# Performance work log

Hardware: AMD Instinct MI355X
Metric: run time of the kernel (lower is better)

Reference implementation:

```python
import jax, jax.numpy as jnp
import numpy as np

NUM_CLASSES = 80
IOU_THR = 0.5
SCORE_THR = 0.3
K = 256              # per-class candidate pool (pre-NMS top-k)
MAX_PER_CLASS = 100  # max_output_size_per_class
MAX_TOTAL = 100      # max_total_size
NEG = -1e9


def _make_boxes(key, shape):
    kc, ks = jax.random.split(key)
    cyx = jax.random.uniform(kc, shape + (2,), dtype=jnp.float32)
    hw = jax.random.uniform(ks, shape + (2,), dtype=jnp.float32) * 0.2
    return jnp.concatenate([cyx - hw * 0.5, cyx + hw * 0.5], axis=-1)  # [y1,x1,y2,x2]


def setup_inputs() -> dict:
    key = jax.random.key(0)
    ks = jax.random.split(key, 9)
    B = 8
    inp = {}
    for i, g in enumerate([52, 26, 13]):
        inp[f"b{i+1}"] = _make_boxes(ks[3 * i], (B, g, g, 3))                       # (B,g,g,3,4)
        inp[f"c{i+1}"] = jax.random.uniform(ks[3 * i + 1], (B, g, g, 3, 1))          # objectness
        inp[f"p{i+1}"] = jax.random.uniform(ks[3 * i + 2], (B, g, g, 3, NUM_CLASSES))
    return inp


def _pairwise_iou(b):  # b: (K,4) in [y1,x1,y2,x2]
    y1, x1, y2, x2 = b[:, 0], b[:, 1], b[:, 2], b[:, 3]
    area = (y2 - y1) * (x2 - x1)
    iy = jnp.clip(jnp.minimum(y2[:, None], y2[None, :]) - jnp.maximum(y1[:, None], y1[None, :]), 0.0)
    ix = jnp.clip(jnp.minimum(x2[:, None], x2[None, :]) - jnp.maximum(x1[:, None], x1[None, :]), 0.0)
    inter = iy * ix
    union = area[:, None] + area[None, :] - inter
    return jnp.where(union > 0, inter / union, 0.0)


def _nms_one_class(boxes, scores):  # boxes (N,4), scores (N,)
    sc, idx = jax.lax.top_k(scores, K)
    b = boxes[idx]                      # (K,4) sorted by score desc
    valid = sc > SCORE_THR
    iou = _pairwise_iou(b)              # (K,K)
    rng = jnp.arange(K)

    def body(keep, i):
        cur = keep[i] & valid[i]
        keep = keep & ~(cur & (iou[i] > IOU_THR) & (rng > i))
        return keep, cur

    _, kept = jax.lax.scan(body, jnp.ones(K, dtype=bool), rng)
    kept = kept & (jnp.cumsum(kept) <= MAX_PER_CLASS)
    return b, jnp.where(kept, sc, NEG)  # (K,4), (K,)


def _combined_nms(boxes, scores):  # boxes (B,N,4), scores (B,N,C)
    per_class = jax.vmap(_nms_one_class, in_axes=(None, 1))   # over classes
    per_image = jax.vmap(per_class, in_axes=(0, 0))           # over batch
    cb, cs = per_image(boxes, scores)                         # (B,C,K,4), (B,C,K)
    B, C = scores.shape[0], scores.shape[2]
    flat_s = cs.reshape(B, C * K)
    flat_b = cb.reshape(B, C * K, 4)
    cls_ids = jnp.broadcast_to(jnp.arange(C, dtype=jnp.float32)[:, None], (C, K)).reshape(C * K)
    top_s, top_i = jax.lax.top_k(flat_s, MAX_TOTAL)           # global top-100
    top_b = jnp.take_along_axis(flat_b, top_i[:, :, None], axis=1)
    top_c = cls_ids[top_i]
    valid = top_s > SCORE_THR
    boxes_out = jnp.clip(jnp.where(valid[..., None], top_b, 0.0), 0.0, 1.0)  # clip_boxes=True
    scores_out = jnp.where(valid, top_s, 0.0)
    classes_out = jnp.where(valid, top_c, 0.0)
    nvalid = valid.sum(axis=-1).astype(jnp.int32)
    return boxes_out, scores_out, classes_out, nvalid


def reference(b1, c1, p1, b2, c2, p2, b3, c3, p3):
    B = b1.shape[0]
    bboxes = jnp.concatenate([b.reshape(B, -1, 4) for b in (b1, b2, b3)], axis=1)          # (B,N,4)
    conf = jnp.concatenate([c.reshape(B, -1, 1) for c in (c1, c2, c3)], axis=1)            # (B,N,1)
    cls = jnp.concatenate([p.reshape(B, -1, NUM_CLASSES) for p in (p1, p2, p3)], axis=1)   # (B,N,C)
    scores = conf * cls                                                                     # (B,N,C)
    return _combined_nms(bboxes, scores)
```

## Files before the change

### kernel.cpp

```cpp
#include <hip/hip_runtime.h>
#include <stdint.h>

#define BATCH 8
#define NC 80
#define NA1 8112
#define NA2 2028
#define NA3 507
#define NTOT 10647
#define TILE 64
#define NTILES 167
#define NSLOTS (NTILES*TILE)
#define KSEL 256
#define MAXPC 100
#define MAXTOT 100
#define SCTHR 0.3f
#define IOUTHR 0.5f
#define KEYTHR 0xBE99999Au
#define KEYBASE 0xBE99999Bu
#define STAGE_CAP 4608

typedef unsigned long long ull;

__device__ ull g_cand[(size_t)BATCH * NC * NSLOTS];
__device__ unsigned g_tcnt[BATCH * NC * NTILES];
__device__ ull g_ks[BATCH * NC * MAXPC];
__device__ unsigned g_kcnt[BATCH * NC];

__device__ __forceinline__ unsigned okey(float f) {
  unsigned u = __float_as_uint(f);
  return u ^ ((unsigned)((int)u >> 31) | 0x80000000u);
}
__device__ __forceinline__ float inv_okey(unsigned k) {
  unsigned u = (k & 0x80000000u) ? (k ^ 0x80000000u) : ~k;
  return __uint_as_float(u);
}
__device__ __forceinline__ ull shflxor64(ull v, int m) {
  int lo = __shfl_xor((int)(unsigned)v, m, 64);
  int hi = __shfl_xor((int)(unsigned)(v >> 32), m, 64);
  return ((ull)(unsigned)hi << 32) | (unsigned)lo;
}
__device__ __forceinline__ ull bcast64(ull v, int src) {
  int lo = __shfl((int)(unsigned)v, src, 64);
  int hi = __shfl((int)(unsigned)(v >> 32), src, 64);
  return ((ull)(unsigned)hi << 32) | (unsigned)lo;
}
__device__ __forceinline__ unsigned wave_sufscan(unsigned v, int lane) {
  #pragma unroll
  for (int off = 1; off < 64; off <<= 1) {
    unsigned t = __shfl_down(v, off, 64);
    if (lane + off < 64) v += t;
  }
  return v;
}

template <typename F>
__device__ void radix_sel24(F getkey, int n, unsigned kwant,
                            unsigned* hist4, unsigned* suf,
                            unsigned* s_sel, unsigned* wtot,
                            unsigned& T_out, unsigned& need_out)
{
  const int tid = threadIdx.x;
  const int lane = tid & 63, wv = tid >> 6;
  const int wb = wv << 8;
  unsigned need = kwant, prefix = 0;
  for (int shift = 16; shift >= 0; shift -= 8) {
    hist4[tid] = 0; hist4[tid + 256] = 0; hist4[tid + 512] = 0; hist4[tid + 768] = 0;
    __syncthreads();
    unsigned maskhi = (shift == 16) ? 0u : (0x00FFFFFFu ^ ((1u << (shift + 8)) - 1u));
    #pragma unroll 4
    for (int i = tid; i < n; i += 256) {
      unsigned k = getkey(i);
      if (k != 0xFFFFFFFFu && (k & maskhi) == prefix)
        atomicAdd(&hist4[wb + ((k >> shift) & 255u)], 1u);
    }
    __syncthreads();
    unsigned v = hist4[tid] + hist4[tid + 256] + hist4[tid + 512] + hist4[tid + 768];
    v = wave_sufscan(v, lane);
    if (lane == 0) wtot[wv] = v;
    __syncthreads();
    unsigned add = 0;
    for (int w = wv + 1; w < 4; ++w) add += wtot[w];
    v += add;
    suf[tid] = v;
    __syncthreads();
    unsigned nxt = (tid == 255) ? 0u : suf[tid + 1];
    if (v >= need && nxt < need) {
      s_sel[0] = prefix | ((unsigned)tid << shift);
      s_sel[1] = need - nxt;
    }
    __syncthreads();
    prefix = s_sel[0]; need = s_sel[1];
    __syncthreads();
  }
  T_out = prefix; need_out = need;
}

__global__ __launch_bounds__(256)
void score_compact(const float* __restrict__ c1, const float* __restrict__ p1,
                   const float* __restrict__ c2, const float* __restrict__ p2,
                   const float* __restrict__ c3, const float* __restrict__ p3)
{
  const int tid = threadIdx.x;
  const int b = blockIdx.x / NTILES;
  const int t = blockIdx.x % NTILES;
  const int n0 = t * TILE;

  __shared__ float sp[TILE * 81];

  for (int e4 = tid; e4 < TILE * 20; e4 += 256) {
    int a = e4 / 20;
    int c4 = (e4 - a * 20) * 4;
    int ng = n0 + a;
    if (ng < NTOT) {
      const float* pp; int nl;
      if (ng < NA1)            { pp = p1 + (size_t)b * NA1 * NC; nl = ng; }
      else if (ng < NA1 + NA2) { pp = p2 + (size_t)b * NA2 * NC; nl = ng - NA1; }
      else                     { pp = p3 + (size_t)b * NA3 * NC; nl = ng - NA1 - NA2; }
      float4 pv = *(const float4*)(pp + (size_t)nl * NC + c4);
      sp[a * 81 + c4 + 0] = pv.x; sp[a * 81 + c4 + 1] = pv.y;
      sp[a * 81 + c4 + 2] = pv.z; sp[a * 81 + c4 + 3] = pv.w;
    }
  }
  __syncthreads();

  const int wv = tid >> 6, lane = tid & 63;
  const int ng = n0 + lane;
  const bool av = ng < NTOT;
  float cf = 0.0f;
  if (av) {
    if (ng < NA1)            cf = c1[b * NA1 + ng];
    else if (ng < NA1 + NA2) cf = c2[b * NA2 + ng - NA1];
    else                     cf = c3[b * NA3 + ng - NA1 - NA2];
  }
  for (int k = 0; k < 20; ++k) {
    int c = wv + 4 * k;
    float pv = av ? sp[lane * 81 + c] : 0.0f;
    unsigned key = okey(pv * cf);
    bool pred = av && (key > KEYTHR);
    ull m = __ballot(pred);
    if (pred) {
      unsigned pos = (unsigned)__popcll(m & ((1ull << lane) - 1ull));
      g_cand[((size_t)(b * NC + c) * NTILES + t) * TILE + pos] =
          ((ull)key << 32) | (unsigned)(~ng);
    }
    if (lane == 0) g_tcnt[(b * NC + c) * NTILES + t] = (unsigned)__popcll(m);
  }
}

__global__ __launch_bounds__(256)
void nms_per_class(const float* __restrict__ b1, const float* __restrict__ b2,
                   const float* __restrict__ b3)
{
  const int tid = threadIdx.x;
  const int lane = tid & 63, wv = tid >> 6;
  const int bc = blockIdx.x;
  const int b = bc / NC;
  const int c = bc - b * NC;

  __shared__ ull cstage[STAGE_CAP];
  __shared__ unsigned tc[NTILES];
  __shared__ unsigned off[NTILES + 1];
  __shared__ unsigned hist4[1024];
  __shared__ unsigned suf[256];
  __shared__ ull cand[KSEL];
  __shared__ ull kw[4], kfw[4];
  __shared__ unsigned s_sel[2], wtot[4];
  __shared__ int s_cgt, s_ceq;
  ull* supp = cstage;
  float4* cbox = (float4*)((char*)cstage + 10240);

  const ull* crow = g_cand + (size_t)bc * NSLOTS;
  const unsigned* trow = g_tcnt + bc * NTILES;

  cand[tid] = 0ull;
  if (tid == 0) { s_cgt = 0; s_ceq = 0; }
  if (tid < NTILES) tc[tid] = trow[tid];
  __syncthreads();

  if (wv == 0) {
    unsigned carry = 0;
    for (int ch = 0; ch < 3; ++ch) {
      int idx = ch * 64 + lane;
      unsigned x = (idx < NTILES) ? tc[idx] : 0u;
      unsigned v = x;
      #pragma unroll
      for (int o = 1; o < 64; o <<= 1) {
        unsigned t2 = __shfl_up(v, o, 64);
        if (lane >= o) v += t2;
      }
      if (idx < NTILES) off[idx] = carry + v - x;
      carry += (unsigned)__shfl((int)v, 63, 64);
    }
    if (lane == 0) off[NTILES] = carry;
  }
  __syncthreads();
  const int cnt = (int)off[NTILES];
  const bool staged = (cnt > KSEL) && (cnt <= STAGE_CAP);

  for (int base = 0; base < NSLOTS; base += 2048) {
    ull v[8]; int pos[8]; bool ok[8];
    #pragma unroll
    for (int e = 0; e < 8; ++e) {
      int s = base + e * 256 + tid;
      ok[e] = false;
      if (s < NSLOTS) {
        int t = s >> 6, j = s & 63;
        if (j < (int)tc[t]) { ok[e] = true; pos[e] = (int)off[t] + j; v[e] = crow[s]; }
      }
    }
    #pragma unroll
    for (int e = 0; e < 8; ++e) {
      if (ok[e]) {
        if (cnt <= KSEL) cand[pos[e]] = v[e];
        else if (staged) cstage[pos[e]] = v[e];
      }
    }
  }
  __syncthreads();

  if (cnt > KSEL) {
    unsigned T, need;
    if (staged) {
      auto gk = [&](int i) { return (unsigned)(cstage[i] >> 32) - KEYBASE; };
      radix_sel24(gk, cnt, KSEL, hist4, suf, s_sel, wtot, T, need);
    } else {
      auto gk = [&](int s) {
        int t = s >> 6, j = s & 63;
        return (j < (int)tc[t]) ? ((unsigned)(crow[s] >> 32) - KEYBASE) : 0xFFFFFFFFu;
      };
      radix_sel24(gk, NSLOTS, KSEL, hist4, suf, s_sel, wtot, T, need);
    }
    const int ngt = KSEL - (int)need;
    if (staged) {
      const int cntPad = (cnt + 255) & ~255;
      for (int i = tid; i < cntPad; i += 256) {
        ull v = (i < cnt) ? cstage[i] : 0ull;
        unsigned k = (unsigned)(v >> 32) - KEYBASE;
        bool g = (i < cnt) && (k > T);
        bool q = (i < cnt) && (k == T);
        ull mg = __ballot(g), mq = __ballot(q);
        unsigned bg = 0, bq = 0;
        if (lane == 0) {
          if (mg) bg = (unsigned)atomicAdd(&s_cgt, (int)__popcll(mg));
          if (mq) bq = (unsigned)atomicAdd(&s_ceq, (int)__popcll(mq));
        }
        bg = (unsigned)__shfl((int)bg, 0, 64);
        bq = (unsigned)__shfl((int)bq, 0, 64);
        ull lt = (1ull << lane) - 1ull;
        if (g) cand[bg + __popcll(mg & lt)] = v;
        if (q) { int p = (int)(bq + __popcll(mq & lt)); if (p < (int)need) cand[ngt + p] = v; }
      }
    } else {
      for (int s = tid; s < NSLOTS; s += 256) {
        int t = s >> 6, j = s & 63;
        if (j < (int)tc[t]) {
          ull v = crow[s];
          unsigned k = (unsigned)(v >> 32) - KEYBASE;
          if (k > T) cand[atomicAdd(&s_cgt, 1)] = v;
          else if (k == T) { int p = atomicAdd(&s_ceq, 1); if (p < (int)need) cand[ngt + p] = v; }
        }
      }
    }
  }
  __syncthreads();

  ull v = cand[tid];
  for (int kk = 2; kk <= KSEL; kk <<= 1) {
    for (int j = kk >> 1; j > 0; j >>= 1) {
      ull o;
      if (j >= 64) {
        cand[tid] = v;
        __syncthreads();
        o = cand[tid ^ j];
        __syncthreads();
      } else {
        o = shflxor64(v, j);
      }
      bool keep_max = (((tid & j) == 0) == ((tid & kk) == 0));
      v = keep_max ? (v > o ? v : o) : (v < o ? v : o);
    }
  }
  __syncthreads();

  {
    float4 bx = make_float4(0.f, 0.f, 0.f, 0.f);
    if (v != 0ull) {
      int myn = (int)(~(unsigned)v);
      const float* bp;
      if (myn < NA1)            bp = b1 + (size_t)(b * NA1 + myn) * 4;
      else if (myn < NA1 + NA2) bp = b2 + (size_t)(b * NA2 + (myn - NA1)) * 4;
      else                      bp = b3 + (size_t)(b * NA3 + (myn - NA1 - NA2)) * 4;
      bx = make_float4(bp[0], bp[1], bp[2], bp[3]);
    }
    cbox[tid] = bx;
  }
  ull mvalid = __ballot(v != 0ull);
  if (lane == 0) kw[wv] = mvalid;
  __syncthreads();

  {
    const float4 mb = cbox[tid];
    const float myarea = (mb.z - mb.x) * (mb.w - mb.y);
    ull m0 = 0, m1 = 0, m2 = 0, m3 = 0;
    #pragma unroll 8
    for (int j = 0; j < KSEL; ++j) {
      float4 bj = cbox[j];
      float ja = (bj.z - bj.x) * (bj.w - bj.y);
      float iy = fmaxf(fminf(bj.z, mb.z) - fmaxf(bj.x, mb.x), 0.0f);
      float ix = fmaxf(fminf(bj.w, mb.w) - fmaxf(bj.y, mb.y), 0.0f);
      float inter = iy * ix;
      float uni = ja + myarea - inter;
      bool sup = (j > tid) && (uni > 0.0f) && (inter > IOUTHR * uni);
      ull bit = sup ? (1ull << (j & 63)) : 0ull;
      if ((j >> 6) == 0) m0 |= bit; else if ((j >> 6) == 1) m1 |= bit;
      else if ((j >> 6) == 2) m2 |= bit; else m3 |= bit;
    }
    supp[tid * 5 + 0] = m0; supp[tid * 5 + 1] = m1;
    supp[tid * 5 + 2] = m2; supp[tid * 5 + 3] = m3;
  }
  __syncthreads();

  if (wv == 0) {
    ull r0[4], r1[4], r2[4], r3[4];
    #pragma unroll
    for (int w = 0; w < 4; ++w) {
      r0[w] = supp[(lane) * 5 + w];
      r1[w] = supp[(64 + lane) * 5 + w];
      r2[w] = supp[(128 + lane) * 5 + w];
      r3[w] = supp[(192 + lane) * 5 + w];
    }
    ull k0 = kw[0], k1 = kw[1], k2 = kw[2], k3 = kw[3];
    ull f0 = 0, f1 = 0, f2 = 0, f3 = 0;
    int run = 0;
#define SCAN_CHUNK(R, KT, FT)                                              \
    if (KT) for (int ib = 0; ib < 64; ++ib) {                              \
      if ((KT >> ib) & 1ull) {                                             \
        k0 &= ~bcast64(R[0], ib); k1 &= ~bcast64(R[1], ib);                \
        k2 &= ~bcast64(R[2], ib); k3 &= ~bcast64(R[3], ib);                \
        FT |= (1ull << ib);                                                \
        if (++run == MAXPC) goto scan_done;                                \
      }                                                                    \
    }
    SCAN_CHUNK(r0, k0, f0)
    SCAN_CHUNK(r1, k1, f1)
    SCAN_CHUNK(r2, k2, f2)
    SCAN_CHUNK(r3, k3, f3)
#undef SCAN_CHUNK
scan_done:
    if (lane == 0) { kfw[0] = f0; kfw[1] = f1; kfw[2] = f2; kfw[3] = f3; }
  }
  __syncthreads();

  {
    ull w0 = kfw[0], w1 = kfw[1], w2 = kfw[2], w3 = kfw[3];
    int wq = tid >> 6, wb2 = tid & 63;
    ull myw = (wq == 0) ? w0 : (wq == 1) ? w1 : (wq == 2) ? w2 : w3;
    bool kept = (myw >> wb2) & 1ull;
    if (kept) {
      ull lt = (wb2 == 0) ? 0ull : (myw & ((1ull << wb2) - 1ull));
      int rank = __popcll(lt);
      if (wq > 0) rank += __popcll(w0);
      if (wq > 1) rank += __popcll(w1);
      if (wq > 2) rank += __popcll(w2);
      unsigned key = (unsigned)(v >> 32);
      unsigned n = (~(unsigned)v) & 0x3FFFu;
      ull e = ((ull)(key - KEYBASE) << 40) | ((ull)(unsigned)(127 - c) << 33) |
              ((ull)(unsigned)(255 - tid) << 25) | n;
      g_ks[(size_t)bc * MAXPC + rank] = e;
    }
    if (tid == 0)
      g_kcnt[bc] = (unsigned)(__popcll(w0) + __popcll(w1) + __popcll(w2) + __popcll(w3));
  }
}

__global__ __launch_bounds__(256)
void nms_final(const float* __restrict__ b1, const float* __restrict__ b2,
               const float* __restrict__ b3, float* __restrict__ out)
{
  const int tid = threadIdx.x;
  const int lane = tid & 63, wv = tid >> 6;
  const int b = blockIdx.x;
  __shared__ ull le[NC * MAXPC];
  __shared__ ull cand[128];
  __shared__ unsigned kc[NC], ko[NC + 1];
  __shared__ unsigned hist4[1024], suf[256], s_sel[2], wtot[4];
  __shared__ int s_cgt, s_ceq;

  if (tid < NC) kc[tid] = g_kcnt[b * NC + tid];
  if (tid < 128) cand[tid] = 0ull;
  if (tid == 0) { s_cgt = 0; s_ceq = 0; }
  __syncthreads();

  if (wv == 0) {
    unsigned carry = 0;
    for (int ch = 0; ch < 2; ++ch) {
      int idx = ch * 64 + lane;
      unsigned x = (idx < NC) ? kc[idx] : 0u;
      unsigned v = x;
      #pragma unroll
      for (int o = 1; o < 64; o <<= 1) {
        unsigned t2 = __shfl_up(v, o, 64);
        if (lane >= o) v += t2;
      }
      if (idx < NC) ko[idx] = carry + v - x;
      carry += (unsigned)__shfl((int)v, 63, 64);
    }
    if (lane == 0) ko[NC] = carry;
  }
  __syncthreads();
  const int total = (int)ko[NC];

  #pragma unroll 4
  for (int s = tid; s < NC * MAXPC; s += 256) {
    int c8 = s / MAXPC, j = s - c8 * MAXPC;
    if (j < (int)kc[c8]) le[ko[c8] + j] = g_ks[(size_t)(b * NC + c8) * MAXPC + j];
  }
  __syncthreads();

  if (total <= MAXTOT) {
    if (tid < total) cand[tid] = le[tid];
  } else {
    unsigned T, need;
    auto gk = [&](int i) { return (unsigned)(le[i] >> 40); };
    radix_sel24(gk, total, MAXTOT, hist4, suf, s_sel, wtot, T, need);
    const int ngt = MAXTOT - (int)need;
    const int totPad = (total + 255) & ~255;
    for (int i = tid; i < totPad; i += 256) {
      ull v = (i < total) ? le[i] : 0ull;
      unsigned k = (unsigned)(v >> 40);
      bool g = (i < total) && (k > T);
      bool q = (i < total) && (k == T);
      ull mg = __ballot(g), mq = __ballot(q);
      unsigned bg = 0, bq = 0;
      if (lane == 0) {
        if (mg) bg = (unsigned)atomicAdd(&s_cgt, (int)__popcll(mg));
        if (mq) bq = (unsigned)atomicAdd(&s_ceq, (int)__popcll(mq));
      }
      bg = (unsigned)__shfl((int)bg, 0, 64);
      bq = (unsigned)__shfl((int)bq, 0, 64);
      ull lt = (1ull << lane) - 1ull;
      if (g) cand[bg + __popcll(mg & lt)] = v;
      if (q) { int p = (int)(bq + __popcll(mq & lt)); if (p < (int)need) cand[ngt + p] = v; }
    }
  }
  __syncthreads();

  for (int kk = 2; kk <= 128; kk <<= 1) {
    for (int j = kk >> 1; j > 0; j >>= 1) {
      if (tid < 128) {
        int ixj = tid ^ j;
        if (ixj > tid) {
          ull a = cand[tid], c2 = cand[ixj];
          if (((tid & kk) == 0) ? (a < c2) : (a > c2)) { cand[tid] = c2; cand[ixj] = a; }
        }
      }
      __syncthreads();
    }
  }

  if (tid < MAXTOT) {
    ull e = cand[tid];
    float o0 = 0.f, o1 = 0.f, o2 = 0.f, o3 = 0.f, osc = 0.f, ocl = 0.f;
    if (e != 0ull) {
      unsigned key24 = (unsigned)(e >> 40);
      float sc = inv_okey(key24 + KEYBASE);
      int cls = 127 - (int)((e >> 33) & 127u);
      int n = (int)(e & 0x3FFFu);
      const float* bp;
      if (n < NA1)            bp = b1 + (size_t)(b * NA1 + n) * 4;
      else if (n < NA1 + NA2) bp = b2 + (size_t)(b * NA2 + (n - NA1)) * 4;
      else                    bp = b3 + (size_t)(b * NA3 + (n - NA1 - NA2)) * 4;
      o0 = fminf(fmaxf(bp[0], 0.0f), 1.0f);
      o1 = fminf(fmaxf(bp[1], 0.0f), 1.0f);
      o2 = fminf(fmaxf(bp[2], 0.0f), 1.0f);
      o3 = fminf(fmaxf(bp[3], 0.0f), 1.0f);
      osc = sc; ocl = (float)cls;
    }
    int oi = b * MAXTOT + tid;
    out[(size_t)oi * 4 + 0] = o0;
    out[(size_t)oi * 4 + 1] = o1;
    out[(size_t)oi * 4 + 2] = o2;
    out[(size_t)oi * 4 + 3] = o3;
    out[BATCH * MAXTOT * 4 + oi] = osc;
    out[BATCH * MAXTOT * 5 + oi] = ocl;
  }
  if (tid == 0) out[BATCH * MAXTOT * 6 + b] = (float)(total < MAXTOT ? total : MAXTOT);
}

extern "C" void kernel_launch(void* const* d_in, const int* in_sizes, int n_in,
                              void* d_out, int out_size, void* d_ws, size_t ws_size,
                              hipStream_t stream) {
  const float* b1 = (const float*)d_in[0];
  const float* c1 = (const float*)d_in[1];
  const float* p1 = (const float*)d_in[2];
  const float* b2 = (const float*)d_in[3];
  const float* c2 = (const float*)d_in[4];
  const float* p2 = (const float*)d_in[5];
  const float* b3 = (const float*)d_in[6];
  const float* c3 = (const float*)d_in[7];
  const float* p3 = (const float*)d_in[8];
  (void)in_sizes; (void)n_in; (void)out_size; (void)d_ws; (void)ws_size;

  score_compact<<<dim3(BATCH * NTILES), dim3(256), 0, stream>>>(c1, p1, c2, p2, c3, p3);
  nms_per_class<<<dim3(BATCH * NC), dim3(256), 0, stream>>>(b1, b2, b3);
  nms_final<<<dim3(BATCH), dim3(256), 0, stream>>>(b1, b2, b3, (float*)d_out);
}
```

Baseline: 227.8 us.

## Replace multi-pass radix select with global histograms and one-pass bucket selection

The score kernel now builds a per-class 256-bucket histogram of candidate keys with global atomics. The per-class NMS kernel uses that histogram to pick a threshold bucket in one scan, and compacts candidates in a single pass with a small rank sort for ties, replacing the three-pass radix select over staged data. The IOU mask loop computes only the lower triangle, the greedy scan uses ballot and find-first-set over alive bits, and kept boxes are scattered into per-image global buckets so the final kernel selects its top 100 via histogram. This adds a zeroing kernel and many global atomics. Capping each final bucket at 128 entries could drop entries if a bucket overflows.

```diff
diff --git a/kernel.cpp b/kernel.cpp
--- a/kernel.cpp
+++ b/kernel.cpp
@@ -17,14 +17,15 @@
 #define IOUTHR 0.5f
 #define KEYTHR 0xBE99999Au
 #define KEYBASE 0xBE99999Bu
-#define STAGE_CAP 4608
+#define CAP2 128
 
 typedef unsigned long long ull;
 
 __device__ ull g_cand[(size_t)BATCH * NC * NSLOTS];
 __device__ unsigned g_tcnt[BATCH * NC * NTILES];
-__device__ ull g_ks[BATCH * NC * MAXPC];
-__device__ unsigned g_kcnt[BATCH * NC];
+__device__ unsigned g_hist[BATCH * NC * 256];
+__device__ ull g_fcand[(size_t)BATCH * 256 * CAP2];
+__device__ unsigned g_fhist[BATCH * 256];
 
 __device__ __forceinline__ unsigned okey(float f) {
   unsigned u = __float_as_uint(f);
@@ -37,11 +38,6 @@
 __device__ __forceinline__ ull shflxor64(ull v, int m) {
   int lo = __shfl_xor((int)(unsigned)v, m, 64);
   int hi = __shfl_xor((int)(unsigned)(v >> 32), m, 64);
-  return ((ull)(unsigned)hi << 32) | (unsigned)lo;
-}
-__device__ __forceinline__ ull bcast64(ull v, int src) {
-  int lo = __shfl((int)(unsigned)v, src, 64);
-  int hi = __shfl((int)(unsigned)(v >> 32), src, 64);
   return ((ull)(unsigned)hi << 32) | (unsigned)lo;
 }
 __device__ __forceinline__ unsigned wave_sufscan(unsigned v, int lane) {
@@ -53,46 +49,10 @@
   return v;
 }
 
-template <typename F>
-__device__ void radix_sel24(F getkey, int n, unsigned kwant,
-                            unsigned* hist4, unsigned* suf,
-                            unsigned* s_sel, unsigned* wtot,
-                            unsigned& T_out, unsigned& need_out)
-{
-  const int tid = threadIdx.x;
-  const int lane = tid & 63, wv = tid >> 6;
-  const int wb = wv << 8;
-  unsigned need = kwant, prefix = 0;
-  for (int shift = 16; shift >= 0; shift -= 8) {
-    hist4[tid] = 0; hist4[tid + 256] = 0; hist4[tid + 512] = 0; hist4[tid + 768] = 0;
-    __syncthreads();
-    unsigned maskhi = (shift == 16) ? 0u : (0x00FFFFFFu ^ ((1u << (shift + 8)) - 1u));
-    #pragma unroll 4
-    for (int i = tid; i < n; i += 256) {
-      unsigned k = getkey(i);
-      if (k != 0xFFFFFFFFu && (k & maskhi) == prefix)
-        atomicAdd(&hist4[wb + ((k >> shift) & 255u)], 1u);
-    }
-    __syncthreads();
-    unsigned v = hist4[tid] + hist4[tid + 256] + hist4[tid + 512] + hist4[tid + 768];
-    v = wave_sufscan(v, lane);
-    if (lane == 0) wtot[wv] = v;
-    __syncthreads();
-    unsigned add = 0;
-    for (int w = wv + 1; w < 4; ++w) add += wtot[w];
-    v += add;
-    suf[tid] = v;
-    __syncthreads();
-    unsigned nxt = (tid == 255) ? 0u : suf[tid + 1];
-    if (v >= need && nxt < need) {
-      s_sel[0] = prefix | ((unsigned)tid << shift);
-      s_sel[1] = need - nxt;
-    }
-    __syncthreads();
-    prefix = s_sel[0]; need = s_sel[1];
-    __syncthreads();
-  }
-  T_out = prefix; need_out = need;
+__global__ void zero_hists() {
+  int i = blockIdx.x * 256 + threadIdx.x;
+  if (i < BATCH * NC * 256) g_hist[i] = 0;
+  if (i < BATCH * 256) g_fhist[i] = 0;
 }
 
 __global__ __launch_bounds__(256)
@@ -142,6 +102,7 @@
       unsigned pos = (unsigned)__popcll(m & ((1ull << lane) - 1ull));
       g_cand[((size_t)(b * NC + c) * NTILES + t) * TILE + pos] =
           ((ull)key << 32) | (unsigned)(~ng);
+      atomicAdd(&g_hist[(b * NC + c) * 256 + ((key - KEYBASE) >> 16)], 1u);
     }
     if (lane == 0) g_tcnt[(b * NC + c) * NTILES + t] = (unsigned)__popcll(m);
   }
@@ -157,109 +118,82 @@
   const int b = bc / NC;
   const int c = bc - b * NC;
 
-  __shared__ ull cstage[STAGE_CAP];
   __shared__ unsigned tc[NTILES];
-  __shared__ unsigned off[NTILES + 1];
-  __shared__ unsigned hist4[1024];
   __shared__ unsigned suf[256];
   __shared__ ull cand[KSEL];
+  __shared__ ull tie[KSEL];
+  __shared__ ull supp[KSEL * 5];
+  __shared__ float4 cbox[KSEL];
   __shared__ ull kw[4], kfw[4];
   __shared__ unsigned s_sel[2], wtot[4];
   __shared__ int s_cgt, s_ceq;
-  ull* supp = cstage;
-  float4* cbox = (float4*)((char*)cstage + 10240);
 
   const ull* crow = g_cand + (size_t)bc * NSLOTS;
-  const unsigned* trow = g_tcnt + bc * NTILES;
 
   cand[tid] = 0ull;
   if (tid == 0) { s_cgt = 0; s_ceq = 0; }
-  if (tid < NTILES) tc[tid] = trow[tid];
-  __syncthreads();
-
-  if (wv == 0) {
-    unsigned carry = 0;
-    for (int ch = 0; ch < 3; ++ch) {
-      int idx = ch * 64 + lane;
-      unsigned x = (idx < NTILES) ? tc[idx] : 0u;
-      unsigned v = x;
-      #pragma unroll
-      for (int o = 1; o < 64; o <<= 1) {
-        unsigned t2 = __shfl_up(v, o, 64);
-        if (lane >= o) v += t2;
-      }
-      if (idx < NTILES) off[idx] = carry + v - x;
-      carry += (unsigned)__shfl((int)v, 63, 64);
-    }
-    if (lane == 0) off[NTILES] = carry;
-  }
-  __syncthreads();
-  const int cnt = (int)off[NTILES];
-  const bool staged = (cnt > KSEL) && (cnt <= STAGE_CAP);
+  if (tid < NTILES) tc[tid] = g_tcnt[bc * NTILES + tid];
+
+  unsigned hv = g_hist[bc * 256 + tid];
+  unsigned v1 = wave_sufscan(hv, lane);
+  if (lane == 0) wtot[wv] = v1;
+  __syncthreads();
+  {
+    unsigned add = 0;
+    for (int w = wv + 1; w < 4; ++w) add += wtot[w];
+    v1 += add;
+  }
+  suf[tid] = v1;
+  __syncthreads();
+  const int total = (int)suf[0];
+  const bool take_all = (total <= KSEL);
+  {
+    unsigned nxt = (tid == 255) ? 0u : suf[tid + 1];
+    if (v1 >= KSEL && nxt < KSEL) { s_sel[0] = (unsigned)tid; s_sel[1] = nxt; }
+  }
+  __syncthreads();
+  const int B1 = take_all ? -1 : (int)s_sel[0];
+  const int n_gt = take_all ? 0 : (int)s_sel[1];
+  const int need1 = KSEL - n_gt;
 
   for (int base = 0; base < NSLOTS; base += 2048) {
-    ull v[8]; int pos[8]; bool ok[8];
+    ull v[8]; bool ok[8];
     #pragma unroll
     for (int e = 0; e < 8; ++e) {
       int s = base + e * 256 + tid;
       ok[e] = false;
       if (s < NSLOTS) {
         int t = s >> 6, j = s & 63;
-        if (j < (int)tc[t]) { ok[e] = true; pos[e] = (int)off[t] + j; v[e] = crow[s]; }
+        if (j < (int)tc[t]) { ok[e] = true; v[e] = crow[s]; }
       }
     }
     #pragma unroll
     for (int e = 0; e < 8; ++e) {
-      if (ok[e]) {
-        if (cnt <= KSEL) cand[pos[e]] = v[e];
-        else if (staged) cstage[pos[e]] = v[e];
+      unsigned bkt = ok[e] ? (((unsigned)(v[e] >> 32) - KEYBASE) >> 16) : 0u;
+      bool toC = ok[e] && (take_all || (int)bkt > B1);
+      bool toT = ok[e] && !take_all && ((int)bkt == B1);
+      ull mg = __ballot(toC), mt = __ballot(toT);
+      unsigned bg = 0, bt = 0;
+      if (lane == 0) {
+        if (mg) bg = (unsigned)atomicAdd(&s_cgt, (int)__popcll(mg));
+        if (mt) bt = (unsigned)atomicAdd(&s_ceq, (int)__popcll(mt));
       }
-    }
-  }
-  __syncthreads();
-
-  if (cnt > KSEL) {
-    unsigned T, need;
-    if (staged) {
-      auto gk = [&](int i) { return (unsigned)(cstage[i] >> 32) - KEYBASE; };
-      radix_sel24(gk, cnt, KSEL, hist4, suf, s_sel, wtot, T, need);
-    } else {
-      auto gk = [&](int s) {
-        int t = s >> 6, j = s & 63;
-        return (j < (int)tc[t]) ? ((unsigned)(crow[s] >> 32) - KEYBASE) : 0xFFFFFFFFu;
-      };
-      radix_sel24(gk, NSLOTS, KSEL, hist4, suf, s_sel, wtot, T, need);
-    }
-    const int ngt = KSEL - (int)need;
-    if (staged) {
-      const int cntPad = (cnt + 255) & ~255;
-      for (int i = tid; i < cntPad; i += 256) {
-        ull v = (i < cnt) ? cstage[i] : 0ull;
-        unsigned k = (unsigned)(v >> 32) - KEYBASE;
-        bool g = (i < cnt) && (k > T);
-        bool q = (i < cnt) && (k == T);
-        ull mg = __ballot(g), mq = __ballot(q);
-        unsigned bg = 0, bq = 0;
-        if (lane == 0) {
-          if (mg) bg = (unsigned)atomicAdd(&s_cgt, (int)__popcll(mg));
-          if (mq) bq = (unsigned)atomicAdd(&s_ceq, (int)__popcll(mq));
-        }
-        bg = (unsigned)__shfl((int)bg, 0, 64);
-        bq = (unsigned)__shfl((int)bq, 0, 64);
-        ull lt = (1ull << lane) - 1ull;
-        if (g) cand[bg + __popcll(mg & lt)] = v;
-        if (q) { int p = (int)(bq + __popcll(mq & lt)); if (p < (int)need) cand[ngt + p] = v; }
-      }
-    } else {
-      for (int s = tid; s < NSLOTS; s += 256) {
-        int t = s >> 6, j = s & 63;
-        if (j < (int)tc[t]) {
-          ull v = crow[s];
-          unsigned k = (unsigned)(v >> 32) - KEYBASE;
-          if (k > T) cand[atomicAdd(&s_cgt, 1)] = v;
-          else if (k == T) { int p = atomicAdd(&s_ceq, 1); if (p < (int)need) cand[ngt + p] = v; }
-        }
-      }
+      bg = (unsigned)__shfl((int)bg, 0, 64);
+      bt = (unsigned)__shfl((int)bt, 0, 64);
+      ull lt = (1ull << lane) - 1ull;
+      if (toC) { unsigned p = bg + (unsigned)__popcll(mg & lt); if (p < KSEL) cand[p] = v[e]; }
+      if (toT) { unsigned p = bt + (unsigned)__popcll(mt & lt); if (p < KSEL) tie[p] = v[e]; }
+    }
+  }
+  __syncthreads();
+
+  {
+    int m = s_ceq < KSEL ? s_ceq : KSEL;
+    if (!take_all && tid < m) {
+      ull e = tie[tid];
+      int rank = 0;
+      for (int i2 = 0; i2 < m; ++i2) rank += (tie[i2] > e) ? 1 : 0;
+      if (rank < need1) cand[n_gt + rank] = e;
     }
   }
   __syncthreads();
@@ -280,12 +214,11 @@
       v = keep_max ? (v > o ? v : o) : (v < o ? v : o);
     }
   }
-  __syncthreads();
 
   {
     float4 bx = make_float4(0.f, 0.f, 0.f, 0.f);
     if (v != 0ull) {
-      int myn = (int)(~(unsigned)v);
+      int myn = (int)(~(unsigned)v) & 0x3FFF;
       const float* bp;
       if (myn < NA1)            bp = b1 + (size_t)(b * NA1 + myn) * 4;
       else if (myn < NA1 + NA2) bp = b2 + (size_t)(b * NA2 + (myn - NA1)) * 4;
@@ -302,15 +235,14 @@
     const float4 mb = cbox[tid];
     const float myarea = (mb.z - mb.x) * (mb.w - mb.y);
     ull m0 = 0, m1 = 0, m2 = 0, m3 = 0;
-    #pragma unroll 8
-    for (int j = 0; j < KSEL; ++j) {
+    for (int j = 0; j < tid; ++j) {
       float4 bj = cbox[j];
       float ja = (bj.z - bj.x) * (bj.w - bj.y);
       float iy = fmaxf(fminf(bj.z, mb.z) - fmaxf(bj.x, mb.x), 0.0f);
       float ix = fmaxf(fminf(bj.w, mb.w) - fmaxf(bj.y, mb.y), 0.0f);
       float inter = iy * ix;
       float uni = ja + myarea - inter;
-      bool sup = (j > tid) && (uni > 0.0f) && (inter > IOUTHR * uni);
+      bool sup = (uni > 0.0f) && (inter > IOUTHR * uni);
       ull bit = sup ? (1ull << (j & 63)) : 0ull;
       if ((j >> 6) == 0) m0 |= bit; else if ((j >> 6) == 1) m1 |= bit;
       else if ((j >> 6) == 2) m2 |= bit; else m3 |= bit;
@@ -321,55 +253,52 @@
   __syncthreads();
 
   if (wv == 0) {
-    ull r0[4], r1[4], r2[4], r3[4];
+    ull colw[4][4];
     #pragma unroll
-    for (int w = 0; w < 4; ++w) {
-      r0[w] = supp[(lane) * 5 + w];
-      r1[w] = supp[(64 + lane) * 5 + w];
-      r2[w] = supp[(128 + lane) * 5 + w];
-      r3[w] = supp[(192 + lane) * 5 + w];
-    }
-    ull k0 = kw[0], k1 = kw[1], k2 = kw[2], k3 = kw[3];
-    ull f0 = 0, f1 = 0, f2 = 0, f3 = 0;
+    for (int q = 0; q < 4; ++q)
+      #pragma unroll
+      for (int w = 0; w < 4; ++w)
+        colw[q][w] = supp[(q * 64 + lane) * 5 + w];
+    bool alive[4], kept[4];
+    #pragma unroll
+    for (int q = 0; q < 4; ++q) {
+      alive[q] = (kw[q] >> lane) & 1ull;
+      kept[q] = false;
+    }
     int run = 0;
-#define SCAN_CHUNK(R, KT, FT)                                              \
-    if (KT) for (int ib = 0; ib < 64; ++ib) {                              \
-      if ((KT >> ib) & 1ull) {                                             \
-        k0 &= ~bcast64(R[0], ib); k1 &= ~bcast64(R[1], ib);                \
-        k2 &= ~bcast64(R[2], ib); k3 &= ~bcast64(R[3], ib);                \
-        FT |= (1ull << ib);                                                \
-        if (++run == MAXPC) goto scan_done;                                \
-      }                                                                    \
-    }
-    SCAN_CHUNK(r0, k0, f0)
-    SCAN_CHUNK(r1, k1, f1)
-    SCAN_CHUNK(r2, k2, f2)
-    SCAN_CHUNK(r3, k3, f3)
-#undef SCAN_CHUNK
-scan_done:
-    if (lane == 0) { kfw[0] = f0; kfw[1] = f1; kfw[2] = f2; kfw[3] = f3; }
-  }
-  __syncthreads();
-
-  {
-    ull w0 = kfw[0], w1 = kfw[1], w2 = kfw[2], w3 = kfw[3];
-    int wq = tid >> 6, wb2 = tid & 63;
-    ull myw = (wq == 0) ? w0 : (wq == 1) ? w1 : (wq == 2) ? w2 : w3;
-    bool kept = (myw >> wb2) & 1ull;
+    for (int w2 = 0; w2 < 4 && run < MAXPC; ++w2) {
+      ull A = __ballot(alive[w2]);
+      while (A != 0ull && run < MAXPC) {
+        int ib = __ffsll((long long)A) - 1;
+        if (lane == ib) kept[w2] = true;
+        ++run;
+        if (run >= MAXPC) break;
+        #pragma unroll
+        for (int q = 0; q < 4; ++q)
+          alive[q] = alive[q] && !((colw[q][w2] >> ib) & 1ull);
+        A = __ballot(alive[w2]);
+        A = (ib >= 63) ? 0ull : (A & ~((2ull << ib) - 1ull));
+      }
+    }
+    #pragma unroll
+    for (int q = 0; q < 4; ++q) {
+      ull f = __ballot(kept[q]);
+      if (lane == 0) kfw[q] = f;
+    }
+  }
+  __syncthreads();
+
+  {
+    bool kept = (kfw[tid >> 6] >> (tid & 63)) & 1ull;
     if (kept) {
-      ull lt = (wb2 == 0) ? 0ull : (myw & ((1ull << wb2) - 1ull));
-      int rank = __popcll(lt);
-      if (wq > 0) rank += __popcll(w0);
-      if (wq > 1) rank += __popcll(w1);
-      if (wq > 2) rank += __popcll(w2);
-      unsigned key = (unsigned)(v >> 32);
+      unsigned key24 = (unsigned)(v >> 32) - KEYBASE;
       unsigned n = (~(unsigned)v) & 0x3FFFu;
-      ull e = ((ull)(key - KEYBASE) << 40) | ((ull)(unsigned)(127 - c) << 33) |
+      ull e = ((ull)key24 << 40) | ((ull)(unsigned)(127 - c) << 33) |
               ((ull)(unsigned)(255 - tid) << 25) | n;
-      g_ks[(size_t)bc * MAXPC + rank] = e;
-    }
-    if (tid == 0)
-      g_kcnt[bc] = (unsigned)(__popcll(w0) + __popcll(w1) + __popcll(w2) + __popcll(w3));
+      unsigned bkt = key24 >> 16;
+      unsigned p = atomicAdd(&g_fhist[b * 256 + bkt], 1u);
+      if (p < CAP2) g_fcand[(size_t)(b * 256 + bkt) * CAP2 + p] = e;
+    }
   }
 }
 
@@ -380,67 +309,59 @@
   const int tid = threadIdx.x;
   const int lane = tid & 63, wv = tid >> 6;
   const int b = blockIdx.x;
-  __shared__ ull le[NC * MAXPC];
   __shared__ ull cand[128];
-  __shared__ unsigned kc[NC], ko[NC + 1];
-  __shared__ unsigned hist4[1024], suf[256], s_sel[2], wtot[4];
-  __shared__ int s_cgt, s_ceq;
-
-  if (tid < NC) kc[tid] = g_kcnt[b * NC + tid];
+  __shared__ ull tie[CAP2];
+  __shared__ unsigned suf[256];
+  __shared__ unsigned s_sel[2], wtot[4];
+  __shared__ int s_cgt, s_mt;
+
   if (tid < 128) cand[tid] = 0ull;
-  if (tid == 0) { s_cgt = 0; s_ceq = 0; }
-  __syncthreads();
-
-  if (wv == 0) {
-    unsigned carry = 0;
-    for (int ch = 0; ch < 2; ++ch) {
-      int idx = ch * 64 + lane;
-      unsigned x = (idx < NC) ? kc[idx] : 0u;
-      unsigned v = x;
-      #pragma unroll
-      for (int o = 1; o < 64; o <<= 1) {
-        unsigned t2 = __shfl_up(v, o, 64);
-        if (lane >= o) v += t2;
-      }
-      if (idx < NC) ko[idx] = carry + v - x;
-      carry += (unsigned)__shfl((int)v, 63, 64);
-    }
-    if (lane == 0) ko[NC] = carry;
-  }
-  __syncthreads();
-  const int total = (int)ko[NC];
-
-  #pragma unroll 4
-  for (int s = tid; s < NC * MAXPC; s += 256) {
-    int c8 = s / MAXPC, j = s - c8 * MAXPC;
-    if (j < (int)kc[c8]) le[ko[c8] + j] = g_ks[(size_t)(b * NC + c8) * MAXPC + j];
-  }
-  __syncthreads();
-
-  if (total <= MAXTOT) {
-    if (tid < total) cand[tid] = le[tid];
-  } else {
-    unsigned T, need;
-    auto gk = [&](int i) { return (unsigned)(le[i] >> 40); };
-    radix_sel24(gk, total, MAXTOT, hist4, suf, s_sel, wtot, T, need);
-    const int ngt = MAXTOT - (int)need;
-    const int totPad = (total + 255) & ~255;
-    for (int i = tid; i < totPad; i += 256) {
-      ull v = (i < total) ? le[i] : 0ull;
-      unsigned k = (unsigned)(v >> 40);
-      bool g = (i < total) && (k > T);
-      bool q = (i < total) && (k == T);
-      ull mg = __ballot(g), mq = __ballot(q);
-      unsigned bg = 0, bq = 0;
-      if (lane == 0) {
-        if (mg) bg = (unsigned)atomicAdd(&s_cgt, (int)__popcll(mg));
-        if (mq) bq = (unsigned)atomicAdd(&s_ceq, (int)__popcll(mq));
-      }
-      bg = (unsigned)__shfl((int)bg, 0, 64);
-      bq = (unsigned)__shfl((int)bq, 0, 64);
-      ull lt = (1ull << lane) - 1ull;
-      if (g) cand[bg + __popcll(mg & lt)] = v;
-      if (q) { int p = (int)(bq + __popcll(mq & lt)); if (p < (int)need) cand[ngt + p] = v; }
+  if (tid == 0) { s_cgt = 0; s_mt = 0; }
+  unsigned h = g_fhist[b * 256 + tid];
+  if (h > CAP2) h = CAP2;
+  unsigned v1 = wave_sufscan(h, lane);
+  if (lane == 0) wtot[wv] = v1;
+  __syncthreads();
+  {
+    unsigned add = 0;
+    for (int w = wv + 1; w < 4; ++w) add += wtot[w];
+    v1 += add;
+  }
+  suf[tid] = v1;
+  __syncthreads();
+  const int total = (int)suf[0];
+  const bool take_all = (total <= MAXTOT);
+  {
+    unsigned nxt = (tid == 255) ? 0u : suf[tid + 1];
+    if (v1 >= MAXTOT && nxt < MAXTOT) { s_sel[0] = (unsigned)tid; s_sel[1] = nxt; }
+  }
+  __syncthreads();
+  const int B1 = take_all ? -1 : (int)s_sel[0];
+  const int n_gt = take_all ? 0 : (int)s_sel[1];
+  const int need = MAXTOT - n_gt;
+
+  {
+    int cnt_t = (int)h;
+    bool mine = (cnt_t > 0) && (take_all || tid > B1);
+    int base = 0;
+    if (mine) base = atomicAdd(&s_cgt, cnt_t);
+    if (mine)
+      for (int i = 0; i < cnt_t; ++i)
+        cand[base + i] = g_fcand[(size_t)(b * 256 + tid) * CAP2 + i];
+    if (!take_all && tid == B1) {
+      s_mt = cnt_t;
+      for (int i = 0; i < cnt_t; ++i)
+        tie[i] = g_fcand[(size_t)(b * 256 + tid) * CAP2 + i];
+    }
+  }
+  __syncthreads();
+  {
+    int m = s_mt;
+    if (tid < m) {
+      ull e = tie[tid];
+      int rank = 0;
+      for (int i2 = 0; i2 < m; ++i2) rank += (tie[i2] > e) ? 1 : 0;
+      if (rank < need) cand[n_gt + rank] = e;
     }
   }
   __syncthreads();
@@ -501,6 +422,7 @@
   const float* p3 = (const float*)d_in[8];
   (void)in_sizes; (void)n_in; (void)out_size; (void)d_ws; (void)ws_size;
 
+  zero_hists<<<dim3((BATCH * NC * 256 + 255) / 256), dim3(256), 0, stream>>>();
   score_compact<<<dim3(BATCH * NTILES), dim3(256), 0, stream>>>(c1, p1, c2, p2, c3, p3);
   nms_per_class<<<dim3(BATCH * NC), dim3(256), 0, stream>>>(b1, b2, b3);
   nms_final<<<dim3(BATCH), dim3(256), 0, stream>>>(b1, b2, b3, (float*)d_out);
```

After: 300.8 us. 32.1% more time.

## Replace three-pass radix select with single-pass bucket select plus tie ranking

Applied to the files above, without the earlier changes.

The 24-bit three-pass radix select used to pick the top-256 per class and the top-100 per image is replaced by one 8-bit histogram pass. Elements above the threshold bucket are scattered to positions given by the suffix sum, and ties in the boundary bucket are ranked with an O(m^2) comparison in shared memory. The global candidate loads in the final kernel are batched, and box loads become float4 reads. This removes two histogram passes and their barriers, but a large boundary bucket makes the tie ranking quadratic, and ties beyond the 256 or 512 tie-buffer cap are dropped.

```diff
diff --git a/kernel.cpp b/kernel.cpp
--- a/kernel.cpp
+++ b/kernel.cpp
@@ -53,48 +53,6 @@
   return v;
 }
 
-template <typename F>
-__device__ void radix_sel24(F getkey, int n, unsigned kwant,
-                            unsigned* hist4, unsigned* suf,
-                            unsigned* s_sel, unsigned* wtot,
-                            unsigned& T_out, unsigned& need_out)
-{
-  const int tid = threadIdx.x;
-  const int lane = tid & 63, wv = tid >> 6;
-  const int wb = wv << 8;
-  unsigned need = kwant, prefix = 0;
-  for (int shift = 16; shift >= 0; shift -= 8) {
-    hist4[tid] = 0; hist4[tid + 256] = 0; hist4[tid + 512] = 0; hist4[tid + 768] = 0;
-    __syncthreads();
-    unsigned maskhi = (shift == 16) ? 0u : (0x00FFFFFFu ^ ((1u << (shift + 8)) - 1u));
-    #pragma unroll 4
-    for (int i = tid; i < n; i += 256) {
-      unsigned k = getkey(i);
-      if (k != 0xFFFFFFFFu && (k & maskhi) == prefix)
-        atomicAdd(&hist4[wb + ((k >> shift) & 255u)], 1u);
-    }
-    __syncthreads();
-    unsigned v = hist4[tid] + hist4[tid + 256] + hist4[tid + 512] + hist4[tid + 768];
-    v = wave_sufscan(v, lane);
-    if (lane == 0) wtot[wv] = v;
-    __syncthreads();
-    unsigned add = 0;
-    for (int w = wv + 1; w < 4; ++w) add += wtot[w];
-    v += add;
-    suf[tid] = v;
-    __syncthreads();
-    unsigned nxt = (tid == 255) ? 0u : suf[tid + 1];
-    if (v >= need && nxt < need) {
-      s_sel[0] = prefix | ((unsigned)tid << shift);
-      s_sel[1] = need - nxt;
-    }
-    __syncthreads();
-    prefix = s_sel[0]; need = s_sel[1];
-    __syncthreads();
-  }
-  T_out = prefix; need_out = need;
-}
-
 __global__ __launch_bounds__(256)
 void score_compact(const float* __restrict__ c1, const float* __restrict__ p1,
                    const float* __restrict__ c2, const float* __restrict__ p2,
@@ -163,18 +121,16 @@
   __shared__ unsigned hist4[1024];
   __shared__ unsigned suf[256];
   __shared__ ull cand[KSEL];
+  __shared__ ull tie[KSEL];
   __shared__ ull kw[4], kfw[4];
-  __shared__ unsigned s_sel[2], wtot[4];
-  __shared__ int s_cgt, s_ceq;
+  __shared__ unsigned s_sel[4], wtot[4];
   ull* supp = cstage;
   float4* cbox = (float4*)((char*)cstage + 10240);
 
   const ull* crow = g_cand + (size_t)bc * NSLOTS;
-  const unsigned* trow = g_tcnt + bc * NTILES;
 
   cand[tid] = 0ull;
-  if (tid == 0) { s_cgt = 0; s_ceq = 0; }
-  if (tid < NTILES) tc[tid] = trow[tid];
+  if (tid < NTILES) tc[tid] = g_tcnt[bc * NTILES + tid];
   __syncthreads();
 
   if (wv == 0) {
@@ -195,7 +151,8 @@
   }
   __syncthreads();
   const int cnt = (int)off[NTILES];
-  const bool staged = (cnt > KSEL) && (cnt <= STAGE_CAP);
+  const bool take_all = (cnt <= KSEL);
+  const bool staged = !take_all && (cnt <= STAGE_CAP);
 
   for (int base = 0; base < NSLOTS; base += 2048) {
     ull v[8]; int pos[8]; bool ok[8];
@@ -211,58 +168,85 @@
     #pragma unroll
     for (int e = 0; e < 8; ++e) {
       if (ok[e]) {
-        if (cnt <= KSEL) cand[pos[e]] = v[e];
+        if (take_all) cand[pos[e]] = v[e];
         else if (staged) cstage[pos[e]] = v[e];
       }
     }
   }
   __syncthreads();
 
-  if (cnt > KSEL) {
-    unsigned T, need;
+  if (!take_all) {
+    hist4[tid] = 0; hist4[tid + 256] = 0; hist4[tid + 512] = 0; hist4[tid + 768] = 0;
+    __syncthreads();
+    const int wb = wv << 8;
     if (staged) {
-      auto gk = [&](int i) { return (unsigned)(cstage[i] >> 32) - KEYBASE; };
-      radix_sel24(gk, cnt, KSEL, hist4, suf, s_sel, wtot, T, need);
+      for (int i = tid; i < cnt; i += 256)
+        atomicAdd(&hist4[wb + ((((unsigned)(cstage[i] >> 32)) - KEYBASE) >> 16)], 1u);
     } else {
-      auto gk = [&](int s) {
+      for (int s = tid; s < NSLOTS; s += 256) {
         int t = s >> 6, j = s & 63;
-        return (j < (int)tc[t]) ? ((unsigned)(crow[s] >> 32) - KEYBASE) : 0xFFFFFFFFu;
-      };
-      radix_sel24(gk, NSLOTS, KSEL, hist4, suf, s_sel, wtot, T, need);
-    }
-    const int ngt = KSEL - (int)need;
+        if (j < (int)tc[t])
+          atomicAdd(&hist4[wb + ((((unsigned)(crow[s] >> 32)) - KEYBASE) >> 16)], 1u);
+      }
+    }
+    __syncthreads();
+    unsigned v1 = hist4[tid] + hist4[tid + 256] + hist4[tid + 512] + hist4[tid + 768];
+    v1 = wave_sufscan(v1, lane);
+    if (lane == 0) wtot[wv] = v1;
+    __syncthreads();
+    { unsigned add = 0; for (int w = wv + 1; w < 4; ++w) add += wtot[w]; v1 += add; }
+    suf[tid] = v1;
+    hist4[tid] = 0;
+    __syncthreads();
+    { unsigned nxt = (tid == 255) ? 0u : suf[tid + 1];
+      if (v1 >= KSEL && nxt < KSEL) {
+        s_sel[0] = (unsigned)tid;
+        s_sel[1] = nxt;
+        s_sel[2] = v1 - nxt;
+      } }
+    __syncthreads();
+    const unsigned B1 = s_sel[0];
+    const int n_gt = (int)s_sel[1];
+    const int need = KSEL - n_gt;
     if (staged) {
-      const int cntPad = (cnt + 255) & ~255;
-      for (int i = tid; i < cntPad; i += 256) {
-        ull v = (i < cnt) ? cstage[i] : 0ull;
-        unsigned k = (unsigned)(v >> 32) - KEYBASE;
-        bool g = (i < cnt) && (k > T);
-        bool q = (i < cnt) && (k == T);
-        ull mg = __ballot(g), mq = __ballot(q);
-        unsigned bg = 0, bq = 0;
-        if (lane == 0) {
-          if (mg) bg = (unsigned)atomicAdd(&s_cgt, (int)__popcll(mg));
-          if (mq) bq = (unsigned)atomicAdd(&s_ceq, (int)__popcll(mq));
+      for (int i = tid; i < cnt; i += 256) {
+        ull v = cstage[i];
+        unsigned bkt = (((unsigned)(v >> 32)) - KEYBASE) >> 16;
+        if (bkt > B1) {
+          unsigned above = (bkt == 255u) ? 0u : suf[bkt + 1];
+          unsigned p = above + atomicAdd(&hist4[bkt], 1u);
+          if (p < KSEL) cand[p] = v;
+        } else if (bkt == B1) {
+          unsigned p = atomicAdd(&hist4[bkt], 1u);
+          if (p < KSEL) tie[p] = v;
         }
-        bg = (unsigned)__shfl((int)bg, 0, 64);
-        bq = (unsigned)__shfl((int)bq, 0, 64);
-        ull lt = (1ull << lane) - 1ull;
-        if (g) cand[bg + __popcll(mg & lt)] = v;
-        if (q) { int p = (int)(bq + __popcll(mq & lt)); if (p < (int)need) cand[ngt + p] = v; }
       }
     } else {
       for (int s = tid; s < NSLOTS; s += 256) {
         int t = s >> 6, j = s & 63;
         if (j < (int)tc[t]) {
           ull v = crow[s];
-          unsigned k = (unsigned)(v >> 32) - KEYBASE;
-          if (k > T) cand[atomicAdd(&s_cgt, 1)] = v;
-          else if (k == T) { int p = atomicAdd(&s_ceq, 1); if (p < (int)need) cand[ngt + p] = v; }
+          unsigned bkt = (((unsigned)(v >> 32)) - KEYBASE) >> 16;
+          if (bkt > B1) {
+            unsigned above = (bkt == 255u) ? 0u : suf[bkt + 1];
+            unsigned p = above + atomicAdd(&hist4[bkt], 1u);
+            if (p < KSEL) cand[p] = v;
+          } else if (bkt == B1) {
+            unsigned p = atomicAdd(&hist4[bkt], 1u);
+            if (p < KSEL) tie[p] = v;
+          }
         }
       }
     }
-  }
-  __syncthreads();
+    __syncthreads();
+    { int m = (int)s_sel[2]; if (m > KSEL) m = KSEL;
+      if (tid < m) {
+        ull e = tie[tid]; int rank = 0;
+        for (int i2 = 0; i2 < m; ++i2) rank += (tie[i2] > e) ? 1 : 0;
+        if (rank < need) cand[n_gt + rank] = e;
+      } }
+    __syncthreads();
+  }
 
   ull v = cand[tid];
   for (int kk = 2; kk <= KSEL; kk <<= 1) {
@@ -285,12 +269,12 @@
   {
     float4 bx = make_float4(0.f, 0.f, 0.f, 0.f);
     if (v != 0ull) {
-      int myn = (int)(~(unsigned)v);
+      int myn = (int)(~(unsigned)v) & 0x3FFF;
       const float* bp;
       if (myn < NA1)            bp = b1 + (size_t)(b * NA1 + myn) * 4;
       else if (myn < NA1 + NA2) bp = b2 + (size_t)(b * NA2 + (myn - NA1)) * 4;
       else                      bp = b3 + (size_t)(b * NA3 + (myn - NA1 - NA2)) * 4;
-      bx = make_float4(bp[0], bp[1], bp[2], bp[3]);
+      bx = *(const float4*)bp;
     }
     cbox[tid] = bx;
   }
@@ -362,9 +346,9 @@
       if (wq > 0) rank += __popcll(w0);
       if (wq > 1) rank += __popcll(w1);
       if (wq > 2) rank += __popcll(w2);
-      unsigned key = (unsigned)(v >> 32);
+      unsigned key24 = (unsigned)(v >> 32) - KEYBASE;
       unsigned n = (~(unsigned)v) & 0x3FFFu;
-      ull e = ((ull)(key - KEYBASE) << 40) | ((ull)(unsigned)(127 - c) << 33) |
+      ull e = ((ull)key24 << 40) | ((ull)(unsigned)(127 - c) << 33) |
               ((ull)(unsigned)(255 - tid) << 25) | n;
       g_ks[(size_t)bc * MAXPC + rank] = e;
     }
@@ -382,13 +366,13 @@
   const int b = blockIdx.x;
   __shared__ ull le[NC * MAXPC];
   __shared__ ull cand[128];
+  __shared__ ull tie[512];
   __shared__ unsigned kc[NC], ko[NC + 1];
-  __shared__ unsigned hist4[1024], suf[256], s_sel[2], wtot[4];
-  __shared__ int s_cgt, s_ceq;
+  __shared__ unsigned hist4[1024], suf[256];
+  __shared__ unsigned s_sel[4], wtot[4];
 
   if (tid < NC) kc[tid] = g_kcnt[b * NC + tid];
   if (tid < 128) cand[tid] = 0ull;
-  if (tid == 0) { s_cgt = 0; s_ceq = 0; }
   __syncthreads();
 
   if (wv == 0) {
@@ -409,41 +393,78 @@
   }
   __syncthreads();
   const int total = (int)ko[NC];
-
-  #pragma unroll 4
-  for (int s = tid; s < NC * MAXPC; s += 256) {
-    int c8 = s / MAXPC, j = s - c8 * MAXPC;
-    if (j < (int)kc[c8]) le[ko[c8] + j] = g_ks[(size_t)(b * NC + c8) * MAXPC + j];
-  }
-  __syncthreads();
-
-  if (total <= MAXTOT) {
+  const bool take_all = (total <= MAXTOT);
+
+  const ull* krow = g_ks + (size_t)b * NC * MAXPC;
+  for (int base = 0; base < NC * MAXPC; base += 2048) {
+    ull v[8]; int pos[8]; bool ok[8];
+    #pragma unroll
+    for (int e = 0; e < 8; ++e) {
+      int s = base + e * 256 + tid;
+      ok[e] = false;
+      if (s < NC * MAXPC) {
+        int cc = s / MAXPC, j = s - cc * MAXPC;
+        if (j < (int)kc[cc]) { ok[e] = true; pos[e] = (int)ko[cc] + j; v[e] = krow[s]; }
+      }
+    }
+    #pragma unroll
+    for (int e = 0; e < 8; ++e)
+      if (ok[e]) le[pos[e]] = v[e];
+  }
+  __syncthreads();
+
+  if (take_all) {
     if (tid < total) cand[tid] = le[tid];
+    __syncthreads();
   } else {
-    unsigned T, need;
-    auto gk = [&](int i) { return (unsigned)(le[i] >> 40); };
-    radix_sel24(gk, total, MAXTOT, hist4, suf, s_sel, wtot, T, need);
-    const int ngt = MAXTOT - (int)need;
-    const int totPad = (total + 255) & ~255;
-    for (int i = tid; i < totPad; i += 256) {
-      ull v = (i < total) ? le[i] : 0ull;
-      unsigned k = (unsigned)(v >> 40);
-      bool g = (i < total) && (k > T);
-      bool q = (i < total) && (k == T);
-      ull mg = __ballot(g), mq = __ballot(q);
-      unsigned bg = 0, bq = 0;
-      if (lane == 0) {
-        if (mg) bg = (unsigned)atomicAdd(&s_cgt, (int)__popcll(mg));
-        if (mq) bq = (unsigned)atomicAdd(&s_ceq, (int)__popcll(mq));
-      }
-      bg = (unsigned)__shfl((int)bg, 0, 64);
-      bq = (unsigned)__shfl((int)bq, 0, 64);
-      ull lt = (1ull << lane) - 1ull;
-      if (g) cand[bg + __popcll(mg & lt)] = v;
-      if (q) { int p = (int)(bq + __popcll(mq & lt)); if (p < (int)need) cand[ngt + p] = v; }
-    }
-  }
-  __syncthreads();
+    hist4[tid] = 0; hist4[tid + 256] = 0; hist4[tid + 512] = 0; hist4[tid + 768] = 0;
+    __syncthreads();
+    const int wb = wv << 8;
+    for (int i = tid; i < total; i += 256)
+      atomicAdd(&hist4[wb + (unsigned)(le[i] >> 56)], 1u);
+    __syncthreads();
+    unsigned v1 = hist4[tid] + hist4[tid + 256] + hist4[tid + 512] + hist4[tid + 768];
+    v1 = wave_sufscan(v1, lane);
+    if (lane == 0) wtot[wv] = v1;
+    __syncthreads();
+    { unsigned add = 0; for (int w = wv + 1; w < 4; ++w) add += wtot[w]; v1 += add; }
+    suf[tid] = v1;
+    hist4[tid] = 0;
+    __syncthreads();
+    { unsigned nxt = (tid == 255) ? 0u : suf[tid + 1];
+      if (v1 >= MAXTOT && nxt < MAXTOT) {
+        s_sel[0] = (unsigned)tid; s_sel[1] = nxt; s_sel[2] = v1 - nxt;
+      } }
+    __syncthreads();
+    const unsigned B1 = s_sel[0];
+    const int n_gt = (int)s_sel[1];
+    const int need = MAXTOT - n_gt;
+    for (int i = tid; i < total; i += 256) {
+      ull v = le[i];
+      unsigned bkt = (unsigned)(v >> 56);
+      if (bkt > B1) {
+        unsigned above = (bkt == 255u) ? 0u : suf[bkt + 1];
+        unsigned p = above + atomicAdd(&hist4[bkt], 1u);
+        if (p < 128u) cand[p] = v;
+      } else if (bkt == B1) {
+        unsigned p = atomicAdd(&hist4[bkt], 1u);
+        if (p < 512u) tie[p] = v;
+      }
+    }
+    __syncthreads();
+    { int m = (int)s_sel[2]; if (m > 512) m = 512;
+      if (tid < m) {
+        ull e = tie[tid]; int rank = 0;
+        for (int i2 = 0; i2 < m; ++i2) rank += (tie[i2] > e) ? 1 : 0;
+        if (rank < need) cand[n_gt + rank] = e;
+      }
+      for (int i = 256 + tid; i < m; i += 256) {
+        ull e = tie[i]; int rank = 0;
+        for (int i2 = 0; i2 < m; ++i2) rank += (tie[i2] > e) ? 1 : 0;
+        if (rank < need) cand[n_gt + rank] = e;
+      } }
+    __syncthreads();
+  }
 
   for (int kk = 2; kk <= 128; kk <<= 1) {
     for (int j = kk >> 1; j > 0; j >>= 1) {
@@ -470,10 +491,11 @@
       if (n < NA1)            bp = b1 + (size_t)(b * NA1 + n) * 4;
       else if (n < NA1 + NA2) bp = b2 + (size_t)(b * NA2 + (n - NA1)) * 4;
       else                    bp = b3 + (size_t)(b * NA3 + (n - NA1 - NA2)) * 4;
-      o0 = fminf(fmaxf(bp[0], 0.0f), 1.0f);
-      o1 = fminf(fmaxf(bp[1], 0.0f), 1.0f);
-      o2 = fminf(fmaxf(bp[2], 0.0f), 1.0f);
-      o3 = fminf(fmaxf(bp[3], 0.0f), 1.0f);
+      float4 bx = *(const float4*)bp;
+      o0 = fminf(fmaxf(bx.x, 0.0f), 1.0f);
+      o1 = fminf(fmaxf(bx.y, 0.0f), 1.0f);
+      o2 = fminf(fmaxf(bx.z, 0.0f), 1.0f);
+      o3 = fminf(fmaxf(bx.w, 0.0f), 1.0f);
       osc = sc; ocl = (float)cls;
     }
     int oi = b * MAXTOT + tid;
```

Result: faster. 218.8 us (-3.9%).
